# Performance work log

Hardware: AMD Instinct MI355X
Metric: run time of the kernel (lower is better)

## Reference

```python
import jax, jax.numpy as jnp
import numpy as np
import math

DIM = 1024
H = 16
DH = DIM // H
B = 2
L = 1024


def setup_inputs() -> dict:
    key = jax.random.key(0)
    ks = jax.random.split(key, 8)
    s = 1.0 / math.sqrt(DIM)
    return {
        "Q": jax.random.normal(ks[0], (B, L, DIM), jnp.float32),
        "K": jax.random.normal(ks[1], (B, L, DIM), jnp.float32),
        "mask_Q": jax.random.bernoulli(ks[2], 0.1, (B, L)),
        "mask_K": jax.random.bernoulli(ks[3], 0.1, (B, L)),
        "Wq": jax.random.normal(ks[4], (DIM, DIM), jnp.float32) * s,
        "Wk": jax.random.normal(ks[5], (DIM, DIM), jnp.float32) * s,
        "Wv": jax.random.normal(ks[6], (DIM, DIM), jnp.float32) * s,
        "Wo": jax.random.normal(ks[7], (DIM, DIM), jnp.float32) * s,
    }


def reference(Q, K, mask_Q, mask_K, Wq, Wk, Wv, Wo):
    # V defaults to K. Masked positions of inputs are zeroed first.
    Qz = jnp.where(mask_Q[:, :, None], 0.0, Q)
    Kz = jnp.where(mask_K[:, :, None], 0.0, K)
    Vz = Kz  # V = K, masked with mask_K

    # Projections (nn.Linear, no bias): y = x @ W.T
    Qp = jnp.einsum('bld,ed->ble', Qz, Wq)
    Kp = jnp.einsum('bld,ed->ble', Kz, Wk)
    Vp = jnp.einsum('bld,ed->ble', Vz, Wv)

    # split heads: [B, L, H, DH] -> per-head attention
    qh = Qp.reshape(B, L, H, DH)
    kh = Kp.reshape(B, L, H, DH)
    vh = Vp.reshape(B, L, H, DH)

    # NOTE: original scales by sqrt(dim) (full dim), not sqrt(dim_split)
    scores = jnp.einsum('bqhd,bkhd->bhqk', qh, kh) / math.sqrt(DIM)

    # outer-product validity mask: valid iff both q and k positions unmasked
    valid = (~mask_Q)[:, None, :, None] & (~mask_K)[:, None, None, :]  # [B,1,Lq,Lk]
    A = jnp.where(valid, scores, -1e38)
    A = jax.nn.softmax(A, axis=-1)
    A = jnp.where(valid, A, 0.0)

    O = jnp.einsum('bhqk,bkhd->bqhd', A, vh).reshape(B, L, DIM)
    # residual uses the PROJECTED Q (Q was reassigned to fc_q(Q) in torch)
    O = Qp + O
    # masked_forward(fc_o, ...): fc_o applied, masked query rows forced to 0
    ff = jax.nn.relu(jnp.where(mask_Q[:, :, None], 0.0, jnp.einsum('bld,ed->ble', O, Wo)))
    O = O + ff
    return O
```

## Files before the change

kernel.cpp:

```cpp
#include <hip/hip_runtime.h>
#include <hip/hip_bf16.h>


#define DEV __device__ __forceinline__

typedef __attribute__((ext_vector_type(8))) short bf16x8;
typedef __attribute__((ext_vector_type(4))) float f32x4;
typedef __hip_bfloat16 bf16;

DEV void glds16(const bf16* g, bf16* s) {
  __builtin_amdgcn_global_load_lds(
      (const __attribute__((address_space(1))) void*)g,
      (__attribute__((address_space(3))) void*)s, 16, 0, 0);
}

DEV unsigned short f2bu(float x) {
  __hip_bfloat16 b = __float2bfloat16(x);
  unsigned short u;
  __builtin_memcpy(&u, &b, 2);
  return u;
}

DEV float bu2f(unsigned short u) {
  unsigned int v = (unsigned int)u << 16;
  float f;
  __builtin_memcpy(&f, &v, 4);
  return f;
}

__global__ __launch_bounds__(256) void cast_all(
    const float* __restrict__ Q, const float* __restrict__ K,
    const unsigned char* __restrict__ mq_raw, const unsigned char* __restrict__ mk_raw,
    const float* __restrict__ W0, const float* __restrict__ W1,
    const float* __restrict__ W2, const float* __restrict__ W3,
    bf16* __restrict__ Qz, bf16* __restrict__ Kz,
    bf16* __restrict__ o0, bf16* __restrict__ o1,
    bf16* __restrict__ o2, bf16* __restrict__ o3,
    unsigned char* __restrict__ mqn,
    unsigned long long* __restrict__ qm64, unsigned long long* __restrict__ km64) {
  __shared__ int cnt;
  const int z = blockIdx.z;
  const int t = threadIdx.x;
  if (z < 2) {
    const float* X = z ? K : Q;
    const unsigned char* raw = z ? mk_raw : mq_raw;
    bf16* out = z ? Kz : Qz;
    if (t == 0) cnt = 0;
    __syncthreads();
    int c = 0;
#pragma unroll
    for (int j = 0; j < 8; ++j) c += (raw[t * 8 + j] != 0);
    atomicAdd(&cnt, c);
    __syncthreads();
    const bool isByte = cnt > 128;
    int i = (blockIdx.x * 256 + t) * 8;
    int row = i >> 10;
    bool masked = isByte ? (raw[row] != 0) : (((const int*)raw)[row] != 0);
    float4 v0 = *(const float4*)&X[i];
    float4 v1 = *(const float4*)&X[i + 4];
    if (masked) {
      v0 = make_float4(0.f, 0.f, 0.f, 0.f);
      v1 = make_float4(0.f, 0.f, 0.f, 0.f);
    }
    *(ushort4*)&out[i] = make_ushort4(f2bu(v0.x), f2bu(v0.y), f2bu(v0.z), f2bu(v0.w));
    *(ushort4*)&out[i + 4] = make_ushort4(f2bu(v1.x), f2bu(v1.y), f2bu(v1.z), f2bu(v1.w));
  } else if (z < 6) {
    if (blockIdx.x >= 512) return;
    const float* X; bf16* out;
    switch (z) {
      case 2: X = W0; out = o0; break;
      case 3: X = W1; out = o1; break;
      case 4: X = W2; out = o2; break;
      default: X = W3; out = o3; break;
    }
    int i = (blockIdx.x * 256 + t) * 8;
    float4 v0 = *(const float4*)&X[i];
    float4 v1 = *(const float4*)&X[i + 4];
    *(ushort4*)&out[i] = make_ushort4(f2bu(v0.x), f2bu(v0.y), f2bu(v0.z), f2bu(v0.w));
    *(ushort4*)&out[i + 4] = make_ushort4(f2bu(v1.x), f2bu(v1.y), f2bu(v1.z), f2bu(v1.w));
  } else {
    if (blockIdx.x != 0) return;
    if (t == 0) cnt = 0;
    __syncthreads();
    int c = 0;
    for (int i = t; i < 2048; i += 256) c += (mq_raw[i] != 0);
    atomicAdd(&cnt, c);
    __syncthreads();
    const bool isByte = cnt > 128;
    for (int i = t; i < 2048; i += 256)
      mqn[i] = isByte ? (mq_raw[i] != 0) : (((const int*)mq_raw)[i] != 0);
    if (t < 64) {
      const unsigned char* src = (t < 32) ? mk_raw : mq_raw;
      int idx = t & 31;
      unsigned long long m = 0;
      for (int j = 0; j < 64; ++j) {
        int pos = idx * 64 + j;
        bool bit = isByte ? (src[pos] != 0) : (((const int*)src)[pos] != 0);
        m |= (unsigned long long)bit << j;
      }
      if (t < 32) km64[idx] = m; else qm64[idx] = m;
    }
  }
}

template <int MI, int NI, typename EPI>
DEV void gemm_core(const bf16* __restrict__ A, const bf16* __restrict__ W,
                   int K, int brow, int bcol, EPI&& epi) {
  __shared__ bf16 As[2 * MI * 512];
  __shared__ bf16 Bs[2 * NI * 2048];
  const int t = threadIdx.x, l = t & 63, w = t >> 6;
  const int rs = l >> 2;
  const int kcol = (l & 3) * 8;

  f32x4 acc[MI][NI];
#pragma unroll
  for (int i = 0; i < MI; i++)
#pragma unroll
    for (int j = 0; j < NI; j++) acc[i][j] = (f32x4){0.f, 0.f, 0.f, 0.f};

  auto stage = [&](int k0, int b_) {
#pragma unroll
    for (int i = 0; i < MI; ++i)
      if ((i & 3) == w)
        glds16(A + (size_t)(brow + i * 16 + rs) * K + k0 + kcol,
               &As[b_ * MI * 512 + i * 512]);
#pragma unroll
    for (int c = 0; c < NI; ++c)
      glds16(W + (size_t)(bcol + (w * NI + c) * 16 + rs) * K + k0 + kcol,
             &Bs[b_ * NI * 2048 + (w * NI + c) * 512]);
  };

  const int aoff0 = (l & 15) * 32 + (l >> 4) * 8;
  const int boff0 = (w * NI * 16 + (l & 15)) * 32 + (l >> 4) * 8;

  stage(0, 0);
  int buf = 0;
  for (int k0 = 0; k0 < K; k0 += 32) {
    __syncthreads();
    if (k0 + 32 < K) stage(k0 + 32, buf ^ 1);
    bf16x8 a[MI], b[NI];
#pragma unroll
    for (int mi = 0; mi < MI; ++mi)
      a[mi] = *(const bf16x8*)&As[buf * MI * 512 + aoff0 + mi * 512];
#pragma unroll
    for (int ni = 0; ni < NI; ++ni)
      b[ni] = *(const bf16x8*)&Bs[buf * NI * 2048 + boff0 + ni * 512];
#pragma unroll
    for (int mi = 0; mi < MI; ++mi)
#pragma unroll
      for (int ni = 0; ni < NI; ++ni)
        acc[mi][ni] = __builtin_amdgcn_mfma_f32_16x16x32_bf16(a[mi], b[ni], acc[mi][ni], 0, 0, 0);
    buf ^= 1;
  }

#pragma unroll
  for (int mi = 0; mi < MI; ++mi)
#pragma unroll
    for (int ni = 0; ni < NI; ++ni)
#pragma unroll
      for (int r = 0; r < 4; ++r) {
        int row = brow + mi * 16 + (l >> 4) * 4 + r;
        int col = bcol + (w * NI + ni) * 16 + (l & 15);
        epi(row, col, acc[mi][ni][r]);
      }
}

__global__ __launch_bounds__(256) void proj_gemm(
    const bf16* __restrict__ Qz, const bf16* __restrict__ Kz,
    const bf16* __restrict__ Wq, const bf16* __restrict__ Wk, const bf16* __restrict__ Wv,
    bf16* __restrict__ Qpb, bf16* __restrict__ Kpb, bf16* __restrict__ Vpb) {
  const int z = blockIdx.z;
  const int brow = blockIdx.x * 64, bcol = blockIdx.y * 128;
  const bf16* A = (z == 0) ? Qz : Kz;
  const bf16* W = (z == 0) ? Wq : ((z == 1) ? Wk : Wv);
  bf16* dst = (z == 0) ? Qpb : ((z == 1) ? Kpb : Vpb);
  const float scale = (z == 0) ? 0.045084220f : 1.0f;
  gemm_core<4, 2>(A, W, 1024, brow, bcol, [&](int row, int col, float v) {
    dst[((size_t)row << 10) + col] = __float2bfloat16(v * scale);
  });
}

__global__ __launch_bounds__(256) void final_gemm(
    const bf16* __restrict__ Ob, const bf16* __restrict__ Wo,
    float* __restrict__ out, const unsigned char* __restrict__ mq) {
  const int brow = blockIdx.x * 64, bcol = blockIdx.y * 64;
  gemm_core<4, 1>(Ob, Wo, 1024, brow, bcol, [&](int row, int col, float v) {
    size_t idx = ((size_t)row << 10) + col;
    float ff = mq[row] ? 0.f : fmaxf(v, 0.f);
    out[idx] = out[idx] + ff;
  });
}

__global__ __launch_bounds__(256) void attn_fused(
    const bf16* __restrict__ Qpb, const bf16* __restrict__ Kpb, const bf16* __restrict__ Vpb,
    const unsigned long long* __restrict__ qm64, const unsigned long long* __restrict__ km64,
    float* __restrict__ Of, bf16* __restrict__ Ob) {
  __shared__ bf16 Klds[2][2][64 * 64];
  __shared__ bf16 Vt[2][64 * 72];

  const int t = threadIdx.x, l = t & 63, w = t >> 6;
  const int q = l & 15, g = l >> 4;
  const int f = blockIdx.x;
  const int bh = (f & 7) + 8 * ((f >> 3) & 3);
  const int qt = f >> 5;
  const int b = bh >> 4, h = bh & 15;
  const size_t bbase = (size_t)b * 1024;

  const int qg = qt * 64 + w * 16 + q;
  const bf16* qptr = Qpb + (bbase + qg) * 1024 + h * 64 + g * 8;
  const bf16x8 qb0 = *(const bf16x8*)qptr;
  const bf16x8 qb1 = *(const bf16x8*)(qptr + 32);

  float psum = 0.f;
  f32x4 oacc[4];
#pragma unroll
  for (int mf = 0; mf < 4; ++mf) oacc[mf] = (f32x4){0.f, 0.f, 0.f, 0.f};

  const int krow_s = l >> 3;
  const int kcol_s = ((l & 7) ^ krow_s) * 8;
  const int vk0 = 2 * (t & 31);
  const int vdc = t >> 5;

  union U { uint4 v; unsigned short s[8]; };
  U uA0, uA1, uB0, uB1;

  auto stageK = [&](int kt_, int b_, int half) {
#pragma unroll
    for (int c = 0; c < 2; ++c) {
      int cw = w * 2 + c;
      glds16(Kpb + (bbase + kt_ * 64 + cw * 8 + krow_s) * 1024 + h * 64 + kcol_s,
             &Klds[b_][half][cw * 512]);
    }
  };
  auto loadV = [&](int kt_, U& x0, U& x1) {
    const bf16* g0 = Vpb + (bbase + kt_ * 64 + vk0) * 1024 + h * 64 + vdc * 8;
    x0.v = *(const uint4*)g0;
    x1.v = *(const uint4*)(g0 + 1024);
  };
  auto writeVt = [&](int half, U& x0, U& x1) {
#pragma unroll
    for (int j = 0; j < 8; ++j) {
      unsigned int pk = (unsigned int)x0.s[j] | ((unsigned int)x1.s[j] << 16);
      *(unsigned int*)((char*)&Vt[half][0] + (vdc * 8 + j) * 144 + vk0 * 2) = pk;
    }
  };
  auto qk_half = [&](const bf16* Kl, unsigned long long mloc,
                     unsigned int* lo, unsigned int* hi) {
    f32x4 S[4];
#pragma unroll
    for (int mf = 0; mf < 4; ++mf) {
#pragma unroll
      for (int r = 0; r < 4; ++r)
        S[mf][r] = ((mloc >> (mf * 16 + r)) & 1ull) ? -1e30f : 0.f;
      const int row = mf * 16 + q;
      const int rowb = row * 128;
      const bf16x8 ka0 = *(const bf16x8*)((const char*)Kl + rowb + ((g ^ (row & 7)) * 16));
      const bf16x8 ka1 = *(const bf16x8*)((const char*)Kl + rowb + (((g + 4) ^ (row & 7)) * 16));
      S[mf] = __builtin_amdgcn_mfma_f32_16x16x32_bf16(ka0, qb0, S[mf], 0, 0, 0);
      S[mf] = __builtin_amdgcn_mfma_f32_16x16x32_bf16(ka1, qb1, S[mf], 0, 0, 0);
    }
#pragma unroll
    for (int mf = 0; mf < 4; ++mf) {
      float p0 = exp2f(S[mf][0]), p1 = exp2f(S[mf][1]);
      float p2 = exp2f(S[mf][2]), p3 = exp2f(S[mf][3]);
      psum += (p0 + p1) + (p2 + p3);
      lo[mf] = (unsigned int)f2bu(p0) | ((unsigned int)f2bu(p1) << 16);
      hi[mf] = (unsigned int)f2bu(p2) | ((unsigned int)f2bu(p3) << 16);
    }
  };
  const int srcA = ((2 * g) & 3) * 16 + q;
  const int srcB = srcA + 16;
  const bool sel = (g >> 1) & 1;
  auto pv_half = [&](const bf16* Vl, unsigned int* lo, unsigned int* hi) {
#pragma unroll
    for (int ks = 0; ks < 2; ++ks) {
      unsigned int a0 = __shfl(lo[2 * ks], srcA), a1 = __shfl(hi[2 * ks], srcA);
      unsigned int a2 = __shfl(lo[2 * ks], srcB), a3 = __shfl(hi[2 * ks], srcB);
      unsigned int b0 = __shfl(lo[2 * ks + 1], srcA), b1 = __shfl(hi[2 * ks + 1], srcA);
      unsigned int b2 = __shfl(lo[2 * ks + 1], srcB), b3 = __shfl(hi[2 * ks + 1], srcB);
      uint4 pw;
      pw.x = sel ? b0 : a0; pw.y = sel ? b1 : a1;
      pw.z = sel ? b2 : a2; pw.w = sel ? b3 : a3;
      const bf16x8 pa = __builtin_bit_cast(bf16x8, pw);
#pragma unroll
      for (int mf = 0; mf < 4; ++mf) {
        const bf16x8 va = *(const bf16x8*)((const char*)Vl + (mf * 16 + q) * 144 + ks * 64 + g * 16);
        oacc[mf] = __builtin_amdgcn_mfma_f32_16x16x32_bf16(va, pa, oacc[mf], 0, 0, 0);
      }
    }
  };

  stageK(0, 0, 0);
  stageK(1, 0, 1);
  loadV(0, uA0, uA1);
  loadV(1, uB0, uB1);
  int buf = 0;

  for (int p = 0; p < 8; ++p) {
    const unsigned long long mloc0 = km64[b * 16 + 2 * p] >> (4 * g);
    const unsigned long long mloc1 = km64[b * 16 + 2 * p + 1] >> (4 * g);

    __syncthreads();

    writeVt(0, uA0, uA1);
    writeVt(1, uB0, uB1);

    unsigned int lo0[4], hi0[4], lo1[4], hi1[4];
    qk_half(&Klds[buf][0][0], mloc0, lo0, hi0);
    qk_half(&Klds[buf][1][0], mloc1, lo1, hi1);

    __syncthreads();

    if (p < 7) {
      stageK(2 * p + 2, buf ^ 1, 0);
      stageK(2 * p + 3, buf ^ 1, 1);
      loadV(2 * p + 2, uA0, uA1);
      loadV(2 * p + 3, uB0, uB1);
    }

    pv_half(&Vt[0][0], lo0, hi0);
    pv_half(&Vt[1][0], lo1, hi1);
    buf ^= 1;
  }

  psum += __shfl_xor(psum, 16);
  psum += __shfl_xor(psum, 32);

  const unsigned long long qm = qm64[b * 16 + qt];
  const bool qvalid = !((qm >> (w * 16 + q)) & 1ull);
  const float inv = (qvalid && psum > 0.f) ? 1.f / psum : 0.f;
  const float RQ = 22.180709777918f;
#pragma unroll
  for (int mf = 0; mf < 4; ++mf) {
    size_t idx = (bbase + qg) * 1024 + h * 64 + mf * 16 + g * 4;
    ushort4 q4 = *(const ushort4*)&Qpb[idx];
    float4 val;
    val.x = bu2f(q4.x) * RQ + oacc[mf][0] * inv;
    val.y = bu2f(q4.y) * RQ + oacc[mf][1] * inv;
    val.z = bu2f(q4.z) * RQ + oacc[mf][2] * inv;
    val.w = bu2f(q4.w) * RQ + oacc[mf][3] * inv;
    *(float4*)&Of[idx] = val;
    *(ushort4*)&Ob[idx] = make_ushort4(f2bu(val.x), f2bu(val.y), f2bu(val.z), f2bu(val.w));
  }
}

extern "C" void kernel_launch(void* const* d_in, const int* in_sizes, int n_in,
                              void* d_out, int out_size, void* d_ws, size_t ws_size,
                              hipStream_t stream) {
  const float* Q = (const float*)d_in[0];
  const float* K = (const float*)d_in[1];
  const unsigned char* mQraw = (const unsigned char*)d_in[2];
  const unsigned char* mKraw = (const unsigned char*)d_in[3];
  const float* Wq = (const float*)d_in[4];
  const float* Wk = (const float*)d_in[5];
  const float* Wv = (const float*)d_in[6];
  const float* Wo = (const float*)d_in[7];
  float* out = (float*)d_out;

  char* ws = (char*)d_ws;
  const size_t MB = 1024 * 1024;
  bf16* Qz  = (bf16*)(ws + 0);
  bf16* Kz  = (bf16*)(ws + 4 * MB);
  bf16* Wqb = (bf16*)(ws + 8 * MB);
  bf16* Wkb = (bf16*)(ws + 10 * MB);
  bf16* Wvb = (bf16*)(ws + 12 * MB);
  bf16* Wob = (bf16*)(ws + 14 * MB);
  bf16* Qpb = (bf16*)(ws + 16 * MB);
  bf16* Kpb = (bf16*)(ws + 20 * MB);
  bf16* Vpb = (bf16*)(ws + 24 * MB);
  bf16* Ob  = (bf16*)(ws + 28 * MB);
  unsigned char* mqn = (unsigned char*)(ws + 32 * MB);
  unsigned long long* km64 = (unsigned long long*)(ws + 32 * MB + 4096);
  unsigned long long* qm64 = km64 + 32;

  dim3 gc(1024, 1, 7);
  cast_all<<<gc, 256, 0, stream>>>(Q, K, mQraw, mKraw, Wq, Wk, Wv, Wo,
                                   Qz, Kz, Wqb, Wkb, Wvb, Wob, mqn, qm64, km64);

  dim3 gp(32, 8, 3);
  proj_gemm<<<gp, 256, 0, stream>>>(Qz, Kz, Wqb, Wkb, Wvb, Qpb, Kpb, Vpb);

  attn_fused<<<512, 256, 0, stream>>>(Qpb, Kpb, Vpb, qm64, km64, out, Ob);

  dim3 gf(32, 16);
  final_gemm<<<gf, 256, 0, stream>>>(Ob, Wob, out, mqn);
}
```

Measured before the change: 100.6 us.

## Drop fp32 residual write; process one key tile per attention iteration

The attention kernel no longer writes the fp32 residual output. The final GEMM epilogue now reads the residual back from the bf16 copy, removing an fp32 store and an fp32 load. The attention loop also processes one 64-key tile per iteration instead of two, which halves LDS usage and register buffers and may raise occupancy, at the cost of twice as many barriers. Taking the residual from bf16 lowers the precision of the final output.

```diff
diff --git a/kernel.cpp b/kernel.cpp
--- a/kernel.cpp
+++ b/kernel.cpp
@@ -186,17 +186,18 @@
   const int brow = blockIdx.x * 64, bcol = blockIdx.y * 64;
   gemm_core<4, 1>(Ob, Wo, 1024, brow, bcol, [&](int row, int col, float v) {
     size_t idx = ((size_t)row << 10) + col;
+    float res = bu2f(((const unsigned short*)Ob)[idx]);
     float ff = mq[row] ? 0.f : fmaxf(v, 0.f);
-    out[idx] = out[idx] + ff;
+    out[idx] = res + ff;
   });
 }
 
 __global__ __launch_bounds__(256) void attn_fused(
     const bf16* __restrict__ Qpb, const bf16* __restrict__ Kpb, const bf16* __restrict__ Vpb,
     const unsigned long long* __restrict__ qm64, const unsigned long long* __restrict__ km64,
-    float* __restrict__ Of, bf16* __restrict__ Ob) {
-  __shared__ bf16 Klds[2][2][64 * 64];
-  __shared__ bf16 Vt[2][64 * 72];
+    bf16* __restrict__ Ob) {
+  __shared__ bf16 Klds[2][64 * 64];
+  __shared__ bf16 Vt[64 * 72];
 
   const int t = threadIdx.x, l = t & 63, w = t >> 6;
   const int q = l & 15, g = l >> 4;
@@ -221,31 +222,38 @@
   const int vk0 = 2 * (t & 31);
   const int vdc = t >> 5;
 
-  union U { uint4 v; unsigned short s[8]; };
-  U uA0, uA1, uB0, uB1;
-
-  auto stageK = [&](int kt_, int b_, int half) {
+  union { uint4 v; unsigned short s[8]; } u0, u1;
+
+  auto stageK = [&](int kt_, int b_) {
 #pragma unroll
     for (int c = 0; c < 2; ++c) {
       int cw = w * 2 + c;
       glds16(Kpb + (bbase + kt_ * 64 + cw * 8 + krow_s) * 1024 + h * 64 + kcol_s,
-             &Klds[b_][half][cw * 512]);
+             &Klds[b_][cw * 512]);
     }
   };
-  auto loadV = [&](int kt_, U& x0, U& x1) {
+  auto loadV = [&](int kt_) {
     const bf16* g0 = Vpb + (bbase + kt_ * 64 + vk0) * 1024 + h * 64 + vdc * 8;
-    x0.v = *(const uint4*)g0;
-    x1.v = *(const uint4*)(g0 + 1024);
+    u0.v = *(const uint4*)g0;
+    u1.v = *(const uint4*)(g0 + 1024);
   };
-  auto writeVt = [&](int half, U& x0, U& x1) {
+
+  stageK(0, 0);
+  loadV(0);
+  int buf = 0;
+
+  for (int kt = 0; kt < 16; ++kt) {
+    const unsigned long long km = km64[b * 16 + kt];
+    const unsigned long long mloc = km >> (4 * g);
+
+    __syncthreads();
+
 #pragma unroll
     for (int j = 0; j < 8; ++j) {
-      unsigned int pk = (unsigned int)x0.s[j] | ((unsigned int)x1.s[j] << 16);
-      *(unsigned int*)((char*)&Vt[half][0] + (vdc * 8 + j) * 144 + vk0 * 2) = pk;
-    }
-  };
-  auto qk_half = [&](const bf16* Kl, unsigned long long mloc,
-                     unsigned int* lo, unsigned int* hi) {
+      unsigned int pk = (unsigned int)u0.s[j] | ((unsigned int)u1.s[j] << 16);
+      *(unsigned int*)((char*)Vt + (vdc * 8 + j) * 144 + vk0 * 2) = pk;
+    }
+
     f32x4 S[4];
 #pragma unroll
     for (int mf = 0; mf < 4; ++mf) {
@@ -254,11 +262,13 @@
         S[mf][r] = ((mloc >> (mf * 16 + r)) & 1ull) ? -1e30f : 0.f;
       const int row = mf * 16 + q;
       const int rowb = row * 128;
-      const bf16x8 ka0 = *(const bf16x8*)((const char*)Kl + rowb + ((g ^ (row & 7)) * 16));
-      const bf16x8 ka1 = *(const bf16x8*)((const char*)Kl + rowb + (((g + 4) ^ (row & 7)) * 16));
+      const bf16x8 ka0 = *(const bf16x8*)((const char*)&Klds[buf][0] + rowb + ((g ^ (row & 7)) * 16));
+      const bf16x8 ka1 = *(const bf16x8*)((const char*)&Klds[buf][0] + rowb + (((g + 4) ^ (row & 7)) * 16));
       S[mf] = __builtin_amdgcn_mfma_f32_16x16x32_bf16(ka0, qb0, S[mf], 0, 0, 0);
       S[mf] = __builtin_amdgcn_mfma_f32_16x16x32_bf16(ka1, qb1, S[mf], 0, 0, 0);
     }
+
+    unsigned int lo[4], hi[4];
 #pragma unroll
     for (int mf = 0; mf < 4; ++mf) {
       float p0 = exp2f(S[mf][0]), p1 = exp2f(S[mf][1]);
@@ -267,11 +277,17 @@
       lo[mf] = (unsigned int)f2bu(p0) | ((unsigned int)f2bu(p1) << 16);
       hi[mf] = (unsigned int)f2bu(p2) | ((unsigned int)f2bu(p3) << 16);
     }
-  };
-  const int srcA = ((2 * g) & 3) * 16 + q;
-  const int srcB = srcA + 16;
-  const bool sel = (g >> 1) & 1;
-  auto pv_half = [&](const bf16* Vl, unsigned int* lo, unsigned int* hi) {
+
+    __syncthreads();
+
+    if (kt < 15) {
+      stageK(kt + 1, buf ^ 1);
+      loadV(kt + 1);
+    }
+
+    const int srcA = ((2 * g) & 3) * 16 + q;
+    const int srcB = srcA + 16;
+    const bool sel = (g >> 1) & 1;
 #pragma unroll
     for (int ks = 0; ks < 2; ++ks) {
       unsigned int a0 = __shfl(lo[2 * ks], srcA), a1 = __shfl(hi[2 * ks], srcA);
@@ -284,42 +300,10 @@
       const bf16x8 pa = __builtin_bit_cast(bf16x8, pw);
 #pragma unroll
       for (int mf = 0; mf < 4; ++mf) {
-        const bf16x8 va = *(const bf16x8*)((const char*)Vl + (mf * 16 + q) * 144 + ks * 64 + g * 16);
+        const bf16x8 va = *(const bf16x8*)((const char*)Vt + (mf * 16 + q) * 144 + ks * 64 + g * 16);
         oacc[mf] = __builtin_amdgcn_mfma_f32_16x16x32_bf16(va, pa, oacc[mf], 0, 0, 0);
       }
     }
-  };
-
-  stageK(0, 0, 0);
-  stageK(1, 0, 1);
-  loadV(0, uA0, uA1);
-  loadV(1, uB0, uB1);
-  int buf = 0;
-
-  for (int p = 0; p < 8; ++p) {
-    const unsigned long long mloc0 = km64[b * 16 + 2 * p] >> (4 * g);
-    const unsigned long long mloc1 = km64[b * 16 + 2 * p + 1] >> (4 * g);
-
-    __syncthreads();
-
-    writeVt(0, uA0, uA1);
-    writeVt(1, uB0, uB1);
-
-    unsigned int lo0[4], hi0[4], lo1[4], hi1[4];
-    qk_half(&Klds[buf][0][0], mloc0, lo0, hi0);
-    qk_half(&Klds[buf][1][0], mloc1, lo1, hi1);
-
-    __syncthreads();
-
-    if (p < 7) {
-      stageK(2 * p + 2, buf ^ 1, 0);
-      stageK(2 * p + 3, buf ^ 1, 1);
-      loadV(2 * p + 2, uA0, uA1);
-      loadV(2 * p + 3, uB0, uB1);
-    }
-
-    pv_half(&Vt[0][0], lo0, hi0);
-    pv_half(&Vt[1][0], lo1, hi1);
     buf ^= 1;
   }
 
@@ -339,7 +323,6 @@
     val.y = bu2f(q4.y) * RQ + oacc[mf][1] * inv;
     val.z = bu2f(q4.z) * RQ + oacc[mf][2] * inv;
     val.w = bu2f(q4.w) * RQ + oacc[mf][3] * inv;
-    *(float4*)&Of[idx] = val;
     *(ushort4*)&Ob[idx] = make_ushort4(f2bu(val.x), f2bu(val.y), f2bu(val.z), f2bu(val.w));
   }
 }
@@ -380,7 +363,7 @@
   dim3 gp(32, 8, 3);
   proj_gemm<<<gp, 256, 0, stream>>>(Qz, Kz, Wqb, Wkb, Wvb, Qpb, Kpb, Vpb);
 
-  attn_fused<<<512, 256, 0, stream>>>(Qpb, Kpb, Vpb, qm64, km64, out, Ob);
+  attn_fused<<<512, 256, 0, stream>>>(Qpb, Kpb, Vpb, qm64, km64, Ob);
 
   dim3 gf(32, 16);
   final_gemm<<<gf, 256, 0, stream>>>(Ob, Wob, out, mqn);
```

Result: faster. 97.04 us (-3.6%).
